# Optimization experiments

Measured on AMD Instinct MI355X. Metric: run time of the kernel, lower is better.

## Reference

```python
import jax, jax.numpy as jnp
import numpy as np
import math

D_MODEL = 1024
N_HEADS = 16
B, T = 4, 2048


def setup_inputs() -> dict:
    key = jax.random.key(0)
    ks = jax.random.split(key, 10)
    s = 1.0 / math.sqrt(D_MODEL)
    x = jax.random.normal(ks[0], (B, T, D_MODEL), dtype=jnp.float32)
    # causal mask, broadcastable over batch and heads; 0 -> masked
    mask = jnp.tril(jnp.ones((T, T), dtype=jnp.int32))[None, None, :, :]
    w_q = jax.random.normal(ks[1], (D_MODEL, D_MODEL), dtype=jnp.float32) * s
    b_q = jnp.zeros((D_MODEL,), dtype=jnp.float32)
    w_k = jax.random.normal(ks[2], (D_MODEL, D_MODEL), dtype=jnp.float32) * s
    b_k = jnp.zeros((D_MODEL,), dtype=jnp.float32)
    w_v = jax.random.normal(ks[3], (D_MODEL, D_MODEL), dtype=jnp.float32) * s
    b_v = jnp.zeros((D_MODEL,), dtype=jnp.float32)
    w_o = jax.random.normal(ks[4], (D_MODEL, D_MODEL), dtype=jnp.float32) * s
    b_o = jnp.zeros((D_MODEL,), dtype=jnp.float32)
    return {"x": x, "mask": mask, "w_q": w_q, "b_q": b_q, "w_k": w_k,
            "b_k": b_k, "w_v": w_v, "b_v": b_v, "w_o": w_o, "b_o": b_o}


def reference(x, mask, w_q, b_q, w_k, b_k, w_v, b_v, w_o, b_o):
    Bx, Tx, C = x.shape
    H = N_HEADS
    d_k = C // H
    def split_heads(y):  # [B,T,C] -> [B,H,T,d_k]
        return y.reshape(Bx, Tx, H, d_k).transpose(0, 2, 1, 3)
    Q = split_heads(x @ w_q + b_q)
    K = split_heads(x @ w_k + b_k)
    V = split_heads(x @ w_v + b_v)
    scores = jnp.einsum('bhqd,bhkd->bhqk', Q, K) / math.sqrt(d_k)
    scores = jnp.where(mask == 0, jnp.float32(-1e9), scores)
    attn = jax.nn.softmax(scores, axis=-1)
    out = jnp.einsum('bhqk,bhkd->bhqd', attn, V)
    out = out.transpose(0, 2, 1, 3).reshape(Bx, Tx, C)
    return out @ w_o + b_o
```

## Files before the change

### kernel.cpp

```cpp
#include <hip/hip_runtime.h>
#include <stdint.h>

#define D_MODEL 1024
#define NH      16
#define BB      4
#define TT      2048
#define MROWS   (BB * TT)

typedef __attribute__((ext_vector_type(8))) short bf16x8;
typedef __attribute__((ext_vector_type(4))) short bf16x4;
typedef __attribute__((ext_vector_type(4))) float f32x4;

__device__ __forceinline__ unsigned short f2bf(float f) {
    union { float f; unsigned int u; } v; v.f = f;
    unsigned int r = v.u + 0x7fffu + ((v.u >> 16) & 1u);
    return (unsigned short)(r >> 16);
}

__device__ __forceinline__ unsigned short f2bf_fast(float f) {
    union { float f; unsigned int u; } v; v.f = f;
    return (unsigned short)((v.u + 0x8000u) >> 16);
}

__device__ __forceinline__ f32x4 mfma_16x16x16_bf16(bf16x4 a, bf16x4 b, f32x4 c) {
    asm("v_mfma_f32_16x16x16_bf16 %0, %1, %2, %0" : "+v"(c) : "v"(a), "v"(b));
    return c;
}

__device__ __forceinline__ void gload_lds16(const unsigned short* g, unsigned short* l) {
    __builtin_amdgcn_global_load_lds(
        (const __attribute__((address_space(1))) void*)g,
        (__attribute__((address_space(3))) void*)l,
        16, 0, 0);
}

__global__ void prep_kernel(const float* __restrict__ x, unsigned short* __restrict__ xb,
                            const float* __restrict__ wq, const float* __restrict__ wk,
                            const float* __restrict__ wv, const float* __restrict__ wo,
                            unsigned short* tq, unsigned short* tk,
                            unsigned short* tv, unsigned short* to_) {
    if (blockIdx.z == 4) {
        int base = (blockIdx.y * 32 + blockIdx.x) * 2048 + threadIdx.x;
        #pragma unroll
        for (int j = 0; j < 8; ++j) {
            int i = base + j * 256;
            float4 v = ((const float4*)x)[i];
            ushort4 o;
            o.x = f2bf(v.x); o.y = f2bf(v.y); o.z = f2bf(v.z); o.w = f2bf(v.w);
            ((ushort4*)xb)[i] = o;
        }
        return;
    }
    const float* src; unsigned short* dst;
    switch (blockIdx.z) {
        case 0:  src = wq; dst = tq; break;
        case 1:  src = wk; dst = tk; break;
        case 2:  src = wv; dst = tv; break;
        default: src = wo; dst = to_; break;
    }
    __shared__ float tile[32][33];
    int tx = threadIdx.x & 31, ty = threadIdx.x >> 5;
    int k0 = blockIdx.y * 32, n0 = blockIdx.x * 32;
    #pragma unroll
    for (int i = 0; i < 4; ++i)
        tile[ty + i * 8][tx] = src[(k0 + ty + i * 8) * D_MODEL + n0 + tx];
    __syncthreads();
    #pragma unroll
    for (int i = 0; i < 4; ++i)
        dst[(n0 + ty + i * 8) * D_MODEL + k0 + tx] = f2bf(tile[tx][ty + i * 8]);
}

__device__ __forceinline__ void gemm_mainloop(const unsigned short* __restrict__ A,
                                              const unsigned short* __restrict__ Bt,
                                              int m0, int n0,
                                              unsigned short* As, unsigned short* Bs,
                                              f32x4 acc[4][4]) {
    const int tid = threadIdx.x;
    const int lane = tid & 63, wave = tid >> 6;
    const int wm = (wave >> 1) * 64, wn = (wave & 1) * 64;
    const int l15 = lane & 15, quad = lane >> 4;
    const int rx7 = l15 & 7;
    const int srow = tid >> 3;
    const int scol = ((tid & 7) ^ (srow & 7)) * 8;
    const unsigned short* Ag = A + (size_t)(m0 + srow) * D_MODEL + scol;
    const unsigned short* Bg = Bt + (size_t)(n0 + srow) * D_MODEL + scol;
    unsigned short* AsW = As + wave * 512;
    unsigned short* BsW = Bs + wave * 512;
    for (int k0 = 0; k0 < D_MODEL; k0 += 64) {
        __syncthreads();
        #pragma unroll
        for (int p = 0; p < 4; ++p) {
            gload_lds16(Ag + k0 + (size_t)(32 * p) * D_MODEL, AsW + (32 * p) * 64);
            gload_lds16(Bg + k0 + (size_t)(32 * p) * D_MODEL, BsW + (32 * p) * 64);
        }
        __syncthreads();
        #pragma unroll
        for (int kk = 0; kk < 2; ++kk) {
            const int co = ((kk * 4 + quad) ^ rx7) * 8;
            bf16x8 af[4], bfr[4];
            #pragma unroll
            for (int mt = 0; mt < 4; ++mt)
                af[mt] = *(const bf16x8*)(As + (wm + mt * 16 + l15) * 64 + co);
            #pragma unroll
            for (int nt = 0; nt < 4; ++nt)
                bfr[nt] = *(const bf16x8*)(Bs + (wn + nt * 16 + l15) * 64 + co);
            #pragma unroll
            for (int mt = 0; mt < 4; ++mt)
                #pragma unroll
                for (int nt = 0; nt < 4; ++nt)
                    acc[mt][nt] = __builtin_amdgcn_mfma_f32_16x16x32_bf16(af[mt], bfr[nt], acc[mt][nt], 0, 0, 0);
        }
    }
}

__global__ __launch_bounds__(256, 2) void gemm_qkv_kernel(
        const unsigned short* __restrict__ Xb, const unsigned short* __restrict__ Wt,
        const float* __restrict__ bq, const float* __restrict__ bk, const float* __restrict__ bv,
        unsigned short* __restrict__ Qo, unsigned short* __restrict__ Ko,
        unsigned short* __restrict__ VTo) {
    __shared__ unsigned short S[18432];
    unsigned short* As = S;
    unsigned short* Bs = S + 8192;
    int m0 = blockIdx.y * 128, n0 = blockIdx.x * 128;
    f32x4 acc[4][4];
    #pragma unroll
    for (int mt = 0; mt < 4; ++mt)
        #pragma unroll
        for (int nt = 0; nt < 4; ++nt)
            acc[mt][nt] = (f32x4){0.f, 0.f, 0.f, 0.f};
    gemm_mainloop(Xb, Wt, m0, n0, As, Bs, acc);

    const int sel = n0 >> 10;
    const float* bias = (sel == 0) ? bq : (sel == 1) ? bk : bv;
    const float scale = (sel == 0) ? 0.125f * 1.44269504f : 1.f;
    const int tid = threadIdx.x, lane = tid & 63, wave = tid >> 6;
    const int wm = (wave >> 1) * 64, wn = (wave & 1) * 64, l15 = lane & 15, quad = lane >> 4;
    if (sel < 2) {
        unsigned short* Out = (sel == 0) ? Qo : Ko;
        __syncthreads();
        unsigned short* R = S + (wn >> 6) * 9216;
        #pragma unroll
        for (int nt = 0; nt < 4; ++nt) {
            int ln = nt * 16 + l15;
            int col = (n0 + wn + nt * 16 + l15) & 1023;
            float bv_ = bias[col];
            #pragma unroll
            for (int mt = 0; mt < 4; ++mt)
                #pragma unroll
                for (int r = 0; r < 4; ++r) {
                    int lm = wm + mt * 16 + quad * 4 + r;
                    R[lm * 72 + ln] = f2bf((acc[mt][nt][r] + bv_) * scale);
                }
        }
        __syncthreads();
        int hh = tid >> 7, t = tid & 127;
        int h0 = (n0 & 1023) >> 6;
        int b = m0 >> 11, tb = m0 & 2047;
        unsigned short* gp = Out + (size_t)((b * NH + h0 + hh) * TT + tb + t) * 64;
        const unsigned short* lp = S + hh * 9216 + t * 72;
        #pragma unroll
        for (int j = 0; j < 8; ++j)
            *(uint4*)(gp + j * 8) = *(const uint4*)(lp + j * 8);
    } else {
        #pragma unroll
        for (int nt = 0; nt < 4; ++nt) {
            int col = (n0 + wn + nt * 16 + l15) & 1023;
            float bv_ = bias[col];
            int h = col >> 6, dd = col & 63;
            #pragma unroll
            for (int mt = 0; mt < 4; ++mt) {
                int gm0 = m0 + wm + mt * 16 + quad * 4;
                int b = gm0 >> 11, t0 = gm0 & 2047;
                ushort4 o;
                o.x = f2bf(acc[mt][nt][0] + bv_);
                o.y = f2bf(acc[mt][nt][1] + bv_);
                o.z = f2bf(acc[mt][nt][2] + bv_);
                o.w = f2bf(acc[mt][nt][3] + bv_);
                *(ushort4*)&VTo[(((size_t)(b * NH + h) * 16 + (t0 >> 7)) * 64 + dd) * 128 + (t0 & 127)] = o;
            }
        }
    }
}

__global__ __launch_bounds__(256, 2) void gemm_out_kernel(
        const unsigned short* __restrict__ Ob, const unsigned short* __restrict__ Wto,
        const float* __restrict__ bo, float* __restrict__ out) {
    __shared__ unsigned short As[128 * 64], Bs[128 * 64];
    int m0 = blockIdx.y * 128, n0 = blockIdx.x * 128;
    f32x4 acc[4][4];
    #pragma unroll
    for (int mt = 0; mt < 4; ++mt)
        #pragma unroll
        for (int nt = 0; nt < 4; ++nt)
            acc[mt][nt] = (f32x4){0.f, 0.f, 0.f, 0.f};
    gemm_mainloop(Ob, Wto, m0, n0, As, Bs, acc);
    const int tid = threadIdx.x, lane = tid & 63, wave = tid >> 6;
    const int wm = (wave >> 1) * 64, wn = (wave & 1) * 64, l15 = lane & 15, quad = lane >> 4;
    #pragma unroll
    for (int nt = 0; nt < 4; ++nt) {
        int gn = n0 + wn + nt * 16 + l15;
        float bv_ = bo[gn];
        #pragma unroll
        for (int mt = 0; mt < 4; ++mt) {
            #pragma unroll
            for (int r = 0; r < 4; ++r) {
                int gm = m0 + wm + mt * 16 + quad * 4 + r;
                out[(size_t)gm * D_MODEL + gn] = acc[mt][nt][r] + bv_;
            }
        }
    }
}

__global__ __launch_bounds__(256, 4) void flash_kernel(
        const unsigned short* __restrict__ Q, const unsigned short* __restrict__ K,
        const unsigned short* __restrict__ VT, unsigned short* __restrict__ O) {
    __shared__ unsigned short S[16384];
    unsigned short* Kd = S;
    unsigned short* Vd = S + 8192;
    const int n = blockIdx.x;
    const int bh = n & 63;
    const int qt = 15 - (n >> 6);
    const int q0 = qt * 128;
    const int tid = threadIdx.x, lane = tid & 63, wave = tid >> 6;
    const int l15 = lane & 15, quad = lane >> 4;
    const int mbase = wave * 32;
    const unsigned short* Qb = Q + (size_t)bh * (TT * 64) + (size_t)q0 * 64;
    const unsigned short* Kb = K + (size_t)bh * (TT * 64);
    const unsigned short* Vtb = VT + (size_t)bh * (16 * 8192);

    int koff[2], voff[2];
    #pragma unroll
    for (int p = 0; p < 2; ++p) {
        int c = p * 256 + tid;
        int r = c >> 3, s = c & 7;
        koff[p] = r * 64 + ((s ^ (r & 7)) * 8);
        voff[p] = r * 128 + ((s ^ (r & 7)) * 8);
    }
    auto fire = [&](int kt, int buf) {
        const unsigned short* Ksrc = Kb + kt * 4096;
        const unsigned short* Vsrc = Vtb + (kt >> 1) * 8192 + (kt & 1) * 64;
        #pragma unroll
        for (int p = 0; p < 2; ++p) {
            gload_lds16(Ksrc + koff[p], Kd + buf * 4096 + (p * 256 + wave * 64) * 8);
            gload_lds16(Vsrc + voff[p], Vd + buf * 4096 + (p * 256 + wave * 64) * 8);
        }
    };

    bf16x8 qf[2][2];
    #pragma unroll
    for (int mt = 0; mt < 2; ++mt)
        #pragma unroll
        for (int kk = 0; kk < 2; ++kk)
            qf[mt][kk] = *(const bf16x8*)(Qb + (size_t)(mbase + mt * 16 + l15) * 64 + kk * 32 + quad * 8);

    float l_full[2] = {0.f, 0.f};
    f32x4 acc[2][4];
    #pragma unroll
    for (int mt = 0; mt < 2; ++mt)
        #pragma unroll
        for (int nt = 0; nt < 4; ++nt) acc[mt][nt] = (f32x4){0.f, 0.f, 0.f, 0.f};

    fire(0, 0);

    const int nkt = 2 * qt + 2;
    for (int kt = 0; kt < nkt; ++kt) {
        const int p = kt & 1;
        __syncthreads();
        if (kt + 1 < nkt) fire(kt + 1, p ^ 1);
        if (kt * 64 > q0 + mbase + 31) continue;
        const unsigned short* Ksl = Kd + p * 4096;
        const unsigned short* Vsl = Vd + p * 4096;

        f32x4 sf[2][2][2];
        #pragma unroll
        for (int s4 = 0; s4 < 2; ++s4)
            #pragma unroll
            for (int mt = 0; mt < 2; ++mt)
                #pragma unroll
                for (int ntl = 0; ntl < 2; ++ntl) sf[s4][mt][ntl] = (f32x4){0.f, 0.f, 0.f, 0.f};
        __builtin_amdgcn_s_setprio(1);
        #pragma unroll
        for (int s4 = 0; s4 < 2; ++s4)
            #pragma unroll
            for (int kk = 0; kk < 2; ++kk)
                #pragma unroll
                for (int ntl = 0; ntl < 2; ++ntl) {
                    int row = s4 * 32 + ntl * 16 + l15;
                    bf16x8 kf = *(const bf16x8*)&Ksl[row * 64 + (((kk * 4 + quad) ^ (row & 7)) * 8)];
                    #pragma unroll
                    for (int mt = 0; mt < 2; ++mt)
                        sf[s4][mt][ntl] = __builtin_amdgcn_mfma_f32_16x16x32_bf16(kf, qf[mt][kk], sf[s4][mt][ntl], 0, 0, 0);
                }
        __builtin_amdgcn_s_setprio(0);
        if (kt >= 2 * qt) {
            const int kofs = (kt - 2 * qt) * 64;
            #pragma unroll
            for (int s4 = 0; s4 < 2; ++s4)
                #pragma unroll
                for (int mt = 0; mt < 2; ++mt) {
                    int qi = mbase + mt * 16 + l15;
                    #pragma unroll
                    for (int ntl = 0; ntl < 2; ++ntl)
                        #pragma unroll
                        for (int r = 0; r < 4; ++r) {
                            int ki = kofs + s4 * 32 + ntl * 16 + quad * 4 + r;
                            if (ki > qi) sf[s4][mt][ntl][r] = -1e30f;
                        }
                }
        }
        bf16x4 pa[2][2][2];
        #pragma unroll
        for (int s4 = 0; s4 < 2; ++s4) {
            #pragma unroll
            for (int mt = 0; mt < 2; ++mt)
                #pragma unroll
                for (int ntl = 0; ntl < 2; ++ntl) {
                    float p0 = __builtin_amdgcn_exp2f(sf[s4][mt][ntl][0]);
                    float p1 = __builtin_amdgcn_exp2f(sf[s4][mt][ntl][1]);
                    float p2 = __builtin_amdgcn_exp2f(sf[s4][mt][ntl][2]);
                    float p3 = __builtin_amdgcn_exp2f(sf[s4][mt][ntl][3]);
                    l_full[mt] += (p0 + p1) + (p2 + p3);
                    bf16x4 pk;
                    pk[0] = (short)f2bf_fast(p0);
                    pk[1] = (short)f2bf_fast(p1);
                    pk[2] = (short)f2bf_fast(p2);
                    pk[3] = (short)f2bf_fast(p3);
                    pa[s4][mt][ntl] = pk;
                }
            __builtin_amdgcn_s_setprio(1);
            #pragma unroll
            for (int ntl = 0; ntl < 2; ++ntl) {
                #pragma unroll
                for (int ntv = 0; ntv < 4; ++ntv) {
                    int d = ntv * 16 + l15;
                    int cch = s4 * 4 + ntl * 2 + (quad >> 1);
                    bf16x4 vf = *(const bf16x4*)&Vsl[d * 64 + ((cch ^ (d & 7)) * 8) + (quad & 1) * 4];
                    #pragma unroll
                    for (int mt = 0; mt < 2; ++mt)
                        acc[mt][ntv] = mfma_16x16x16_bf16(pa[s4][mt][ntl], vf, acc[mt][ntv]);
                }
            }
            __builtin_amdgcn_s_setprio(0);
        }
    }

    const int b = bh >> 4, h = bh & 15;
    float inv[2][4];
    #pragma unroll
    for (int mt = 0; mt < 2; ++mt) {
        float l = l_full[mt];
        l += __shfl_xor(l, 16);
        l += __shfl_xor(l, 32);
        #pragma unroll
        for (int r = 0; r < 4; ++r) {
            float lr = __shfl(l, quad * 4 + r);
            inv[mt][r] = __builtin_amdgcn_rcpf(lr);
        }
    }
    __syncthreads();
    unsigned short* Ost = S;
    #pragma unroll
    for (int mt = 0; mt < 2; ++mt)
        #pragma unroll
        for (int nt = 0; nt < 4; ++nt)
            #pragma unroll
            for (int r = 0; r < 4; ++r)
                Ost[(mbase + mt * 16 + quad * 4 + r) * 72 + nt * 16 + l15] =
                    f2bf(acc[mt][nt][r] * inv[mt][r]);
    __syncthreads();
    {
        int row = tid >> 1, seg = tid & 1;
        unsigned short* gp = O + (size_t)(b * TT + q0 + row) * D_MODEL + h * 64 + seg * 32;
        const unsigned short* lp = Ost + row * 72 + seg * 32;
        #pragma unroll
        for (int j = 0; j < 4; ++j)
            *(uint4*)(gp + j * 8) = *(const uint4*)(lp + j * 8);
    }
}

extern "C" void kernel_launch(void* const* d_in, const int* in_sizes, int n_in,
                              void* d_out, int out_size, void* d_ws, size_t ws_size,
                              hipStream_t stream) {
    const float* x  = (const float*)d_in[0];
    const float* wq = (const float*)d_in[2];
    const float* bq = (const float*)d_in[3];
    const float* wk = (const float*)d_in[4];
    const float* bk = (const float*)d_in[5];
    const float* wv = (const float*)d_in[6];
    const float* bv = (const float*)d_in[7];
    const float* wo = (const float*)d_in[8];
    const float* bo = (const float*)d_in[9];

    char* ws = (char*)d_ws;
    unsigned short* Xb  = (unsigned short*)ws;
    unsigned short* Wtq = (unsigned short*)(ws + (size_t)(16 << 20));
    unsigned short* Wtk = Wtq + (size_t)D_MODEL * D_MODEL;
    unsigned short* Wtv = Wtk + (size_t)D_MODEL * D_MODEL;
    unsigned short* Wto = Wtv + (size_t)D_MODEL * D_MODEL;
    unsigned short* Qb  = Wto + (size_t)D_MODEL * D_MODEL;
    unsigned short* Kb  = Qb + (size_t)MROWS * D_MODEL;
    unsigned short* VTb = Kb + (size_t)MROWS * D_MODEL;
    unsigned short* Ob  = Xb;

    prep_kernel<<<dim3(32, 32, 5), 256, 0, stream>>>(x, Xb, wq, wk, wv, wo, Wtq, Wtk, Wtv, Wto);
    gemm_qkv_kernel<<<dim3(3 * D_MODEL / 128, MROWS / 128), 256, 0, stream>>>(
        Xb, Wtq, bq, bk, bv, Qb, Kb, VTb);
    flash_kernel<<<dim3(16 * 64), 256, 0, stream>>>(Qb, Kb, VTb, Ob);
    gemm_out_kernel<<<dim3(D_MODEL / 128, MROWS / 128), 256, 0, stream>>>(Ob, Wto, bo, (float*)d_out);
}
```

Baseline: 261.9 us.

## Pair complementary causal query tiles in one 512-thread flash block sharing K/V loads

Each flash block now has 512 threads in two 4-wave groups. One group handles query tile 15-pr and the other handles tile pr, so every block does the same amount of causal work, and the grid is halved. Both groups share the K/V tiles staged into LDS for up to the longer tile's key range, which cuts redundant global K/V traffic and balances load across blocks. In exchange the shorter group sits idle at barriers once its range is done, and the larger block with more LDS may lower occupancy.

```diff
diff --git a/kernel.cpp b/kernel.cpp
--- a/kernel.cpp
+++ b/kernel.cpp
@@ -211,39 +211,31 @@
     }
 }
 
-__global__ __launch_bounds__(256, 4) void flash_kernel(
+__global__ __launch_bounds__(512, 4) void flash_kernel(
         const unsigned short* __restrict__ Q, const unsigned short* __restrict__ K,
         const unsigned short* __restrict__ VT, unsigned short* __restrict__ O) {
-    __shared__ unsigned short S[16384];
+    __shared__ unsigned short S[18432];
     unsigned short* Kd = S;
     unsigned short* Vd = S + 8192;
     const int n = blockIdx.x;
     const int bh = n & 63;
-    const int qt = 15 - (n >> 6);
+    const int pr = n >> 6;
+    const int tid = threadIdx.x, lane = tid & 63, wave = tid >> 6;
+    const int g = wave >> 2;
+    const int qt = g ? pr : (15 - pr);
     const int q0 = qt * 128;
-    const int tid = threadIdx.x, lane = tid & 63, wave = tid >> 6;
     const int l15 = lane & 15, quad = lane >> 4;
-    const int mbase = wave * 32;
+    const int mbase = (wave & 3) * 32;
     const unsigned short* Qb = Q + (size_t)bh * (TT * 64) + (size_t)q0 * 64;
     const unsigned short* Kb = K + (size_t)bh * (TT * 64);
     const unsigned short* Vtb = VT + (size_t)bh * (16 * 8192);
 
-    int koff[2], voff[2];
-    #pragma unroll
-    for (int p = 0; p < 2; ++p) {
-        int c = p * 256 + tid;
-        int r = c >> 3, s = c & 7;
-        koff[p] = r * 64 + ((s ^ (r & 7)) * 8);
-        voff[p] = r * 128 + ((s ^ (r & 7)) * 8);
-    }
+    const int kr = tid >> 3, ks = tid & 7;
+    const int koff = kr * 64 + ((ks ^ (kr & 7)) * 8);
+    const int voff = kr * 128 + ((ks ^ (kr & 7)) * 8);
     auto fire = [&](int kt, int buf) {
-        const unsigned short* Ksrc = Kb + kt * 4096;
-        const unsigned short* Vsrc = Vtb + (kt >> 1) * 8192 + (kt & 1) * 64;
-        #pragma unroll
-        for (int p = 0; p < 2; ++p) {
-            gload_lds16(Ksrc + koff[p], Kd + buf * 4096 + (p * 256 + wave * 64) * 8);
-            gload_lds16(Vsrc + voff[p], Vd + buf * 4096 + (p * 256 + wave * 64) * 8);
-        }
+        gload_lds16(Kb + kt * 4096 + koff, Kd + buf * 4096 + wave * 512);
+        gload_lds16(Vtb + (kt >> 1) * 8192 + (kt & 1) * 64 + voff, Vd + buf * 4096 + wave * 512);
     };
 
     bf16x8 qf[2][2];
@@ -262,7 +254,7 @@
 
     fire(0, 0);
 
-    const int nkt = 2 * qt + 2;
+    const int nkt = 32 - 2 * pr;
     for (int kt = 0; kt < nkt; ++kt) {
         const int p = kt & 1;
         __syncthreads();
@@ -358,7 +350,7 @@
         }
     }
     __syncthreads();
-    unsigned short* Ost = S;
+    unsigned short* Ost = S + g * 9216;
     #pragma unroll
     for (int mt = 0; mt < 2; ++mt)
         #pragma unroll
@@ -370,8 +362,10 @@
     __syncthreads();
     {
         int row = tid >> 1, seg = tid & 1;
-        unsigned short* gp = O + (size_t)(b * TT + q0 + row) * D_MODEL + h * 64 + seg * 32;
-        const unsigned short* lp = Ost + row * 72 + seg * 32;
+        int gg = row >> 7, r128 = row & 127;
+        int qtw = gg ? pr : (15 - pr);
+        unsigned short* gp = O + (size_t)(b * TT + qtw * 128 + r128) * D_MODEL + h * 64 + seg * 32;
+        const unsigned short* lp = S + gg * 9216 + r128 * 72 + seg * 32;
         #pragma unroll
         for (int j = 0; j < 4; ++j)
             *(uint4*)(gp + j * 8) = *(const uint4*)(lp + j * 8);
@@ -405,6 +399,6 @@
     prep_kernel<<<dim3(32, 32, 5), 256, 0, stream>>>(x, Xb, wq, wk, wv, wo, Wtq, Wtk, Wtv, Wto);
     gemm_qkv_kernel<<<dim3(3 * D_MODEL / 128, MROWS / 128), 256, 0, stream>>>(
         Xb, Wtq, bq, bk, bv, Qb, Kb, VTb);
-    flash_kernel<<<dim3(16 * 64), 256, 0, stream>>>(Qb, Kb, VTb, Ob);
+    flash_kernel<<<dim3(8 * 64), 512, 0, stream>>>(Qb, Kb, VTb, Ob);
     gemm_out_kernel<<<dim3(D_MODEL / 128, MROWS / 128), 256, 0, stream>>>(Ob, Wto, bo, (float*)d_out);
 }
```

Measured after the change: 245.8 us. 1.07x faster.
